# Optimization experiments

Measured on AMD Instinct MI355X. Metric: run time of the kernel, lower is better.

Reference implementation:

```python
import jax, jax.numpy as jnp
import numpy as np

DELTA_V = 0.5
DELTA_D = 1.5
ALPHA = 1.0
BETA = 1.0
GAMMA = 0.001
K = 33  # label ids 0..32; 0 = background (ignored)
EPS = 1e-12


def setup_inputs() -> dict:
    key = jax.random.key(0)
    k1, k2 = jax.random.split(key)
    B, N, E = 8, 65536, 32
    embeddings = jax.random.normal(k1, (B, N, E), dtype=jnp.float32)
    labels = jax.random.randint(k2, (B, N), 0, K)
    return {"embeddings": embeddings, "labels": labels}


def reference(embeddings, labels):
    B, N, E = embeddings.shape
    dt = embeddings.dtype
    seg = (labels + jnp.arange(B)[:, None] * K).reshape(-1)  # (B*N,)

    # segment mean -> per-instance centers (B, K, E)
    sums = jax.ops.segment_sum(embeddings.reshape(B * N, E), seg, num_segments=B * K).reshape(B, K, E)
    counts = jax.ops.segment_sum(jnp.ones((B * N,), dtype=dt), seg, num_segments=B * K).reshape(B, K)
    centers = sums / jnp.maximum(counts, 1.0)[..., None]

    present = counts > 0
    present = present.at[:, 0].set(False)  # drop background label 0
    presf = present.astype(dt)
    n_inst = presf.sum(axis=1)  # (B,)

    # ---- variance term: per-point hinge distance to own center, segment-mean ----
    c_per_point = centers[jnp.arange(B)[:, None], labels]  # (B, N, E) gather
    d2 = ((embeddings - c_per_point) ** 2).sum(-1)
    dist = jnp.sqrt(jnp.maximum(d2, EPS))
    hinge = jnp.where(labels > 0, jnp.maximum(dist - DELTA_V, 0.0), 0.0)
    per_inst_sum = jax.ops.segment_sum(hinge.reshape(-1), seg, num_segments=B * K).reshape(B, K)
    per_inst_mean = per_inst_sum / jnp.maximum(counts, 1.0)
    variance_term = (per_inst_mean * presf).sum(1) / jnp.maximum(n_inst, 1.0)

    # ---- distance term: pairwise hinge between present instance centers ----
    diff2 = ((centers[:, :, None, :] - centers[:, None, :, :]) ** 2).sum(-1)  # (B,K,K)
    upper = jnp.triu(jnp.ones((K, K), dtype=bool), 1)[None]
    pair_valid = present[:, :, None] & present[:, None, :] & upper
    cd = jnp.sqrt(jnp.maximum(jnp.where(pair_valid, diff2, 1.0), EPS))
    pair_hinge = jnp.maximum(2.0 * DELTA_D - cd, 0.0) * pair_valid.astype(dt)
    n_pairs = n_inst * (n_inst - 1.0) * 0.5
    distance_term = pair_hinge.sum((1, 2)) / jnp.maximum(n_pairs, 1.0)

    # ---- regularization: mean L2 norm of present centers ----
    c_norm = jnp.sqrt(jnp.maximum((centers ** 2).sum(-1), EPS))
    reg_term = (c_norm * presf).sum(1) / jnp.maximum(n_inst, 1.0)

    per_batch = ALPHA * variance_term + BETA * distance_term + GAMMA * reg_term
    per_batch = jnp.where(n_inst > 0, per_batch, 0.0)
    return per_batch.sum() / B
```

## Files before the change

### kernel.cpp

```cpp
#include <hip/hip_runtime.h>
#include <math.h>

#define KC 33
#define ED 32
#define KE (KC * ED)
#define PAD 33

#define BPB_A 64
#define TPA 128
#define NSLOT 8
#define BPB_H 128
#define TPH 256


__global__ void k_zero(float* __restrict__ ws, int n, float* __restrict__ out) {
    int i = blockIdx.x * blockDim.x + threadIdx.x;
    if (i < n) ws[i] = 0.f;
    if (i == 0) out[0] = 0.f;
}

__global__ __launch_bounds__(256) void k_accum(const float* __restrict__ emb,
                                               const int* __restrict__ lab,
                                               float* __restrict__ sums,
                                               float* __restrict__ counts, int N) {
    __shared__ float s_tile[TPA * PAD];
    __shared__ float s_priv[NSLOT * KE];
    __shared__ int   s_lab[TPA];
    __shared__ float s_hist[2 * KC];
    int t = threadIdx.x;
    for (int i = t; i < NSLOT * KE; i += 256) s_priv[i] = 0.f;
    if (t < 2 * KC) s_hist[t] = 0.f;

    int b     = blockIdx.x / BPB_A;
    int blk   = blockIdx.x % BPB_A;
    int chunk = N / BPB_A;
    int e     = t & 31;
    int slot  = t >> 5;
    size_t pbase = (size_t)b * N + (size_t)blk * chunk;
    const int NT = chunk / TPA;

    const float4* g4 = (const float4*)(emb + pbase * ED);
    float4 r0 = g4[t], r1 = g4[t + 256], r2 = g4[t + 512], r3 = g4[t + 768];
    int rl = 0;
    if (t < TPA) rl = lab[pbase + t];
    __syncthreads();

    for (int tb = 0; tb < NT; tb++) {
        {
            int f, p, m;
            f = t;        p = f >> 3; m = (f & 7) * 4;
            { float* d = &s_tile[PAD * p + m]; d[0]=r0.x; d[1]=r0.y; d[2]=r0.z; d[3]=r0.w; }
            f = t + 256;  p = f >> 3; m = (f & 7) * 4;
            { float* d = &s_tile[PAD * p + m]; d[0]=r1.x; d[1]=r1.y; d[2]=r1.z; d[3]=r1.w; }
            f = t + 512;  p = f >> 3; m = (f & 7) * 4;
            { float* d = &s_tile[PAD * p + m]; d[0]=r2.x; d[1]=r2.y; d[2]=r2.z; d[3]=r2.w; }
            f = t + 768;  p = f >> 3; m = (f & 7) * 4;
            { float* d = &s_tile[PAD * p + m]; d[0]=r3.x; d[1]=r3.y; d[2]=r3.z; d[3]=r3.w; }
        }
        if (t < TPA) {
            s_lab[t] = rl;
            atomicAdd(&s_hist[(t >> 6) * KC + rl], 1.f);
        }
        __syncthreads();

        if (tb + 1 < NT) {
            const float4* gn = (const float4*)(emb + (pbase + (size_t)(tb + 1) * TPA) * ED);
            r0 = gn[t]; r1 = gn[t + 256]; r2 = gn[t + 512]; r3 = gn[t + 768];
            if (t < TPA) rl = lab[pbase + (size_t)(tb + 1) * TPA + t];
        }

        float* priv = &s_priv[slot * KE];
#pragma unroll
        for (int st = 0; st < TPA / NSLOT; st++) {
            int pt = st * NSLOT + slot;
            float x = s_tile[pt * PAD + e];
            int   k = s_lab[pt];
            priv[k * ED + e] += x;
        }
        __syncthreads();
    }

    for (int i = t; i < KE; i += 256) {
        float v = 0.f;
#pragma unroll
        for (int s = 0; s < NSLOT; s++) v += s_priv[s * KE + i];
        atomicAdd(&sums[(size_t)b * KE + i], v);
    }
    if (t < KC)
        atomicAdd(&counts[b * KC + t], s_hist[t] + s_hist[KC + t]);
}

__global__ __launch_bounds__(256) void k_hinge(const float* __restrict__ emb,
                                               const int* __restrict__ lab,
                                               const float* __restrict__ sums,
                                               const float* __restrict__ counts,
                                               float* __restrict__ var,
                                               unsigned* __restrict__ done,
                                               float* __restrict__ out,
                                               int N, int B) {
    __shared__ float s_tile[TPH * PAD];
    __shared__ float s_ctr[KC * PAD];
    __shared__ float s_cnt[KC];
    __shared__ float s_inv[KC];
    __shared__ int   s_prs[KC];
    __shared__ float s_reg[KC];
    __shared__ int   s_lab[TPH];
    __shared__ float s_red[4];
    __shared__ float s_red2[256];
    __shared__ int   s_last;
    int t     = threadIdx.x;
    int b     = blockIdx.x / BPB_H;
    int blk   = blockIdx.x % BPB_H;
    int chunk = N / BPB_H;
    size_t pbase = (size_t)b * N + (size_t)blk * chunk;
    const int NT = chunk / TPH;

    const float4* g4 = (const float4*)(emb + pbase * ED);
    float4 r0 = g4[t],        r1 = g4[t + 256],  r2 = g4[t + 512],  r3 = g4[t + 768];
    float4 r4 = g4[t + 1024], r5 = g4[t + 1280], r6 = g4[t + 1536], r7 = g4[t + 1792];
    int rl = lab[pbase + t];

    if (t < KC) {
        float c = counts[b * KC + t];
        s_cnt[t] = fmaxf(c, 1.f);
        int p = (t > 0 && c > 0.f) ? 1 : 0;
        s_inv[t] = p ? 1.f / fmaxf(c, 1.f) : 0.f;
        s_prs[t] = p;
    }
    __syncthreads();
    for (int i = t; i < KE; i += 256) {
        int k = i >> 5, e = i & 31;
        s_ctr[k * PAD + e] = sums[(size_t)b * KE + i] / s_cnt[k];
    }

    float hs = 0.f;
    for (int tb = 0; tb < NT; tb++) {
        {
            int f, p, m;
            f = t;         p = f >> 3; m = (f & 7) * 4;
            { float* d = &s_tile[PAD * p + m]; d[0]=r0.x; d[1]=r0.y; d[2]=r0.z; d[3]=r0.w; }
            f = t + 256;   p = f >> 3; m = (f & 7) * 4;
            { float* d = &s_tile[PAD * p + m]; d[0]=r1.x; d[1]=r1.y; d[2]=r1.z; d[3]=r1.w; }
            f = t + 512;   p = f >> 3; m = (f & 7) * 4;
            { float* d = &s_tile[PAD * p + m]; d[0]=r2.x; d[1]=r2.y; d[2]=r2.z; d[3]=r2.w; }
            f = t + 768;   p = f >> 3; m = (f & 7) * 4;
            { float* d = &s_tile[PAD * p + m]; d[0]=r3.x; d[1]=r3.y; d[2]=r3.z; d[3]=r3.w; }
            f = t + 1024;  p = f >> 3; m = (f & 7) * 4;
            { float* d = &s_tile[PAD * p + m]; d[0]=r4.x; d[1]=r4.y; d[2]=r4.z; d[3]=r4.w; }
            f = t + 1280;  p = f >> 3; m = (f & 7) * 4;
            { float* d = &s_tile[PAD * p + m]; d[0]=r5.x; d[1]=r5.y; d[2]=r5.z; d[3]=r5.w; }
            f = t + 1536;  p = f >> 3; m = (f & 7) * 4;
            { float* d = &s_tile[PAD * p + m]; d[0]=r6.x; d[1]=r6.y; d[2]=r6.z; d[3]=r6.w; }
            f = t + 1792;  p = f >> 3; m = (f & 7) * 4;
            { float* d = &s_tile[PAD * p + m]; d[0]=r7.x; d[1]=r7.y; d[2]=r7.z; d[3]=r7.w; }
        }
        s_lab[t] = rl;
        __syncthreads();

        if (tb + 1 < NT) {
            const float4* gn = (const float4*)(emb + (pbase + (size_t)(tb + 1) * TPH) * ED);
            r0 = gn[t];        r1 = gn[t + 256];  r2 = gn[t + 512];  r3 = gn[t + 768];
            r4 = gn[t + 1024]; r5 = gn[t + 1280]; r6 = gn[t + 1536]; r7 = gn[t + 1792];
            rl = lab[pbase + (size_t)(tb + 1) * TPH + t];
        }

        int   k  = s_lab[t];
        float iv = s_inv[k];
        const float* xr = &s_tile[t * PAD];
        const float* cr = &s_ctr[k * PAD];
        float d2 = 0.f;
#pragma unroll
        for (int j = 0; j < ED; j++) {
            float d = xr[j] - cr[j];
            d2 = fmaf(d, d, d2);
        }
        float dist = sqrtf(fmaxf(d2, 1e-12f));
        hs += fmaxf(dist - 0.5f, 0.f) * iv;
        __syncthreads();
    }

    hs += __shfl_xor(hs, 1);  hs += __shfl_xor(hs, 2);  hs += __shfl_xor(hs, 4);
    hs += __shfl_xor(hs, 8);  hs += __shfl_xor(hs, 16); hs += __shfl_xor(hs, 32);
    if ((t & 63) == 0) s_red[t >> 6] = hs;
    __syncthreads();
    if (t == 0) {
        atomicAdd(&var[b], s_red[0] + s_red[1] + s_red[2] + s_red[3]);
        __threadfence();
        unsigned old = atomicAdd(&done[b], 1u);
        s_last = (old == (unsigned)(BPB_H - 1)) ? 1 : 0;
    }
    __syncthreads();
    if (!s_last) return;

    __threadfence();
    if (t < KC) {
        float n2 = 0.f;
        for (int e2 = 0; e2 < ED; e2++) { float c = s_ctr[t * PAD + e2]; n2 += c * c; }
        s_reg[t] = s_prs[t] ? sqrtf(fmaxf(n2, 1e-12f)) : 0.f;
    }
    __syncthreads();

    float psum = 0.f;
    for (int q = t; q < KC * KC; q += 256) {
        int i = q / KC, j = q % KC;
        if (i < j && s_prs[i] && s_prs[j]) {
            float d2 = 0.f;
            for (int e2 = 0; e2 < ED; e2++) {
                float d = s_ctr[i * PAD + e2] - s_ctr[j * PAD + e2];
                d2 += d * d;
            }
            float cd = sqrtf(fmaxf(d2, 1e-12f));
            psum += fmaxf(3.0f - cd, 0.f);
        }
    }
    s_red2[t] = psum;
    __syncthreads();
    for (int s = 128; s > 0; s >>= 1) {
        if (t < s) s_red2[t] += s_red2[t + s];
        __syncthreads();
    }

    if (t == 0) {
        float vb = atomicAdd(&var[b], 0.f);
        float reg = 0.f; int n = 0;
        for (int k = 0; k < KC; k++) { reg += s_reg[k]; n += s_prs[k]; }
        float nf = (float)n;
        float variance_term = vb / fmaxf(nf, 1.f);
        float npairs = nf * (nf - 1.f) * 0.5f;
        float distance_term = s_red2[0] / fmaxf(npairs, 1.f);
        float reg_term = reg / fmaxf(nf, 1.f);
        float pb = variance_term + distance_term + 0.001f * reg_term;
        if (n == 0) pb = 0.f;
        atomicAdd(out, pb / (float)B);
    }
}

extern "C" void kernel_launch(void* const* d_in, const int* in_sizes, int n_in,
                              void* d_out, int out_size, void* d_ws, size_t ws_size,
                              hipStream_t stream) {
    const float* emb = (const float*)d_in[0];
    const int*   lab = (const int*)d_in[1];
    float* out = (float*)d_out;

    const int B = 8;
    const int N = in_sizes[1] / B;

    float*    sums   = (float*)d_ws;
    float*    counts = sums + (size_t)B * KE;
    float*    var    = counts + (size_t)B * KC;
    unsigned* done   = (unsigned*)(var + B);

    int zn = B * KE + B * KC + B + B;
    k_zero<<<(zn + 255) / 256, 256, 0, stream>>>((float*)d_ws, zn, out);
    k_accum<<<B * BPB_A, 256, 0, stream>>>(emb, lab, sums, counts, N);
    k_hinge<<<B * BPB_H, 256, 0, stream>>>(emb, lab, sums, counts, var, done, out, N, B);
}
```

Measured before the change: 147.9 us.

## Fuse accumulation and hinge kernels with per-batch grid barrier and reload

Merges the segment-sum kernel and the hinge/loss kernel into one persistent-style kernel. Each block accumulates its chunk, signals a per-batch ready counter, spin-waits until all 64 blocks of that batch finish, then computes the hinge over the same chunk, which it reloads from global memory and which is likely L2-resident. Labels are kept in registers across both phases. This removes one launch and the separate cold pass over the embeddings, but relies on all 512 blocks being co-resident to avoid deadlock and adds spin-wait synchronisation.

```diff
diff --git a/kernel.cpp b/kernel.cpp
--- a/kernel.cpp
+++ b/kernel.cpp
@@ -6,11 +6,11 @@
 #define KE (KC * ED)
 #define PAD 33
 
-#define BPB_A 64
+#define BPB 64
 #define TPA 128
+#define NT 8
 #define NSLOT 8
-#define BPB_H 128
-#define TPH 256
+#define NT2 4
 
 
 __global__ void k_zero(float* __restrict__ ws, int n, float* __restrict__ out) {
@@ -19,30 +19,43 @@
     if (i == 0) out[0] = 0.f;
 }
 
-__global__ __launch_bounds__(256) void k_accum(const float* __restrict__ emb,
-                                               const int* __restrict__ lab,
-                                               float* __restrict__ sums,
-                                               float* __restrict__ counts, int N) {
-    __shared__ float s_tile[TPA * PAD];
+__global__ __launch_bounds__(256, 2) void k_fused(
+        const float* __restrict__ emb, const int* __restrict__ lab,
+        float* __restrict__ sums, float* __restrict__ counts,
+        float* __restrict__ var, unsigned* __restrict__ done,
+        unsigned* __restrict__ ready, float* __restrict__ out,
+        int N, int B) {
+    __shared__ float s_tile[2 * TPA * PAD];
     __shared__ float s_priv[NSLOT * KE];
-    __shared__ int   s_lab[TPA];
     __shared__ float s_hist[2 * KC];
+    __shared__ int   s_lab[2 * TPA];
+    __shared__ float s_ctr[KC * PAD];
+    __shared__ float s_cnt[KC];
+    __shared__ float s_inv[KC];
+    __shared__ int   s_prs[KC];
+    __shared__ float s_reg[KC];
+    __shared__ float s_red[4];
+    __shared__ float s_red2[256];
+    __shared__ int   s_last;
     int t = threadIdx.x;
+    int b = blockIdx.x / BPB;
+    int blk = blockIdx.x % BPB;
+    int chunk = N / BPB;
+    int e = t & 31, slot = t >> 3 >> 2;
+    slot = t >> 5;
+    size_t pbase = (size_t)b * N + (size_t)blk * chunk;
+    const float4* g4 = (const float4*)(emb + pbase * ED);
+
     for (int i = t; i < NSLOT * KE; i += 256) s_priv[i] = 0.f;
     if (t < 2 * KC) s_hist[t] = 0.f;
 
-    int b     = blockIdx.x / BPB_A;
-    int blk   = blockIdx.x % BPB_A;
-    int chunk = N / BPB_A;
-    int e     = t & 31;
-    int slot  = t >> 5;
-    size_t pbase = (size_t)b * N + (size_t)blk * chunk;
-    const int NT = chunk / TPA;
-
-    const float4* g4 = (const float4*)(emb + pbase * ED);
+    int rl_all[NT];
+    if (t < TPA) {
+#pragma unroll
+        for (int tb = 0; tb < NT; tb++) rl_all[tb] = lab[pbase + tb * TPA + t];
+    }
+
     float4 r0 = g4[t], r1 = g4[t + 256], r2 = g4[t + 512], r3 = g4[t + 768];
-    int rl = 0;
-    if (t < TPA) rl = lab[pbase + t];
     __syncthreads();
 
     for (int tb = 0; tb < NT; tb++) {
@@ -58,15 +71,14 @@
             { float* d = &s_tile[PAD * p + m]; d[0]=r3.x; d[1]=r3.y; d[2]=r3.z; d[3]=r3.w; }
         }
         if (t < TPA) {
-            s_lab[t] = rl;
-            atomicAdd(&s_hist[(t >> 6) * KC + rl], 1.f);
+            s_lab[t] = rl_all[tb];
+            atomicAdd(&s_hist[(t >> 6) * KC + rl_all[tb]], 1.f);
         }
         __syncthreads();
 
         if (tb + 1 < NT) {
             const float4* gn = (const float4*)(emb + (pbase + (size_t)(tb + 1) * TPA) * ED);
             r0 = gn[t]; r1 = gn[t + 256]; r2 = gn[t + 512]; r3 = gn[t + 768];
-            if (t < TPA) rl = lab[pbase + (size_t)(tb + 1) * TPA + t];
         }
 
         float* priv = &s_priv[slot * KE];
@@ -74,12 +86,11 @@
         for (int st = 0; st < TPA / NSLOT; st++) {
             int pt = st * NSLOT + slot;
             float x = s_tile[pt * PAD + e];
-            int   k = s_lab[pt];
+            int k = s_lab[pt];
             priv[k * ED + e] += x;
         }
         __syncthreads();
     }
-
     for (int i = t; i < KE; i += 256) {
         float v = 0.f;
 #pragma unroll
@@ -88,40 +99,20 @@
     }
     if (t < KC)
         atomicAdd(&counts[b * KC + t], s_hist[t] + s_hist[KC + t]);
-}
-
-__global__ __launch_bounds__(256) void k_hinge(const float* __restrict__ emb,
-                                               const int* __restrict__ lab,
-                                               const float* __restrict__ sums,
-                                               const float* __restrict__ counts,
-                                               float* __restrict__ var,
-                                               unsigned* __restrict__ done,
-                                               float* __restrict__ out,
-                                               int N, int B) {
-    __shared__ float s_tile[TPH * PAD];
-    __shared__ float s_ctr[KC * PAD];
-    __shared__ float s_cnt[KC];
-    __shared__ float s_inv[KC];
-    __shared__ int   s_prs[KC];
-    __shared__ float s_reg[KC];
-    __shared__ int   s_lab[TPH];
-    __shared__ float s_red[4];
-    __shared__ float s_red2[256];
-    __shared__ int   s_last;
-    int t     = threadIdx.x;
-    int b     = blockIdx.x / BPB_H;
-    int blk   = blockIdx.x % BPB_H;
-    int chunk = N / BPB_H;
-    size_t pbase = (size_t)b * N + (size_t)blk * chunk;
-    const int NT = chunk / TPH;
-
-    const float4* g4 = (const float4*)(emb + pbase * ED);
-    float4 r0 = g4[t],        r1 = g4[t + 256],  r2 = g4[t + 512],  r3 = g4[t + 768];
-    float4 r4 = g4[t + 1024], r5 = g4[t + 1280], r6 = g4[t + 1536], r7 = g4[t + 1792];
-    int rl = lab[pbase + t];
+    __syncthreads();
+
+    if (t == 0) {
+        __threadfence();
+        atomicAdd(&ready[b], 1u);
+        while (__hip_atomic_load(&ready[b], __ATOMIC_ACQUIRE,
+                                 __HIP_MEMORY_SCOPE_AGENT) < (unsigned)BPB)
+            __builtin_amdgcn_s_sleep(8);
+    }
+    __syncthreads();
 
     if (t < KC) {
-        float c = counts[b * KC + t];
+        float c = __hip_atomic_load(&counts[b * KC + t], __ATOMIC_RELAXED,
+                                    __HIP_MEMORY_SCOPE_AGENT);
         s_cnt[t] = fmaxf(c, 1.f);
         int p = (t > 0 && c > 0.f) ? 1 : 0;
         s_inv[t] = p ? 1.f / fmaxf(c, 1.f) : 0.f;
@@ -129,39 +120,46 @@
     }
     __syncthreads();
     for (int i = t; i < KE; i += 256) {
-        int k = i >> 5, e = i & 31;
-        s_ctr[k * PAD + e] = sums[(size_t)b * KE + i] / s_cnt[k];
-    }
+        int k = i >> 5, e2 = i & 31;
+        float sv = __hip_atomic_load(&sums[(size_t)b * KE + i], __ATOMIC_RELAXED,
+                                     __HIP_MEMORY_SCOPE_AGENT);
+        s_ctr[k * PAD + e2] = sv / s_cnt[k];
+    }
+
+    float4 x0 = g4[t],        x1 = g4[t + 256],  x2 = g4[t + 512],  x3 = g4[t + 768];
+    float4 x4 = g4[t + 1024], x5 = g4[t + 1280], x6 = g4[t + 1536], x7 = g4[t + 1792];
 
     float hs = 0.f;
-    for (int tb = 0; tb < NT; tb++) {
+    for (int i2 = 0; i2 < NT2; i2++) {
         {
             int f, p, m;
             f = t;         p = f >> 3; m = (f & 7) * 4;
-            { float* d = &s_tile[PAD * p + m]; d[0]=r0.x; d[1]=r0.y; d[2]=r0.z; d[3]=r0.w; }
+            { float* d = &s_tile[PAD * p + m]; d[0]=x0.x; d[1]=x0.y; d[2]=x0.z; d[3]=x0.w; }
             f = t + 256;   p = f >> 3; m = (f & 7) * 4;
-            { float* d = &s_tile[PAD * p + m]; d[0]=r1.x; d[1]=r1.y; d[2]=r1.z; d[3]=r1.w; }
+            { float* d = &s_tile[PAD * p + m]; d[0]=x1.x; d[1]=x1.y; d[2]=x1.z; d[3]=x1.w; }
             f = t + 512;   p = f >> 3; m = (f & 7) * 4;
-            { float* d = &s_tile[PAD * p + m]; d[0]=r2.x; d[1]=r2.y; d[2]=r2.z; d[3]=r2.w; }
+            { float* d = &s_tile[PAD * p + m]; d[0]=x2.x; d[1]=x2.y; d[2]=x2.z; d[3]=x2.w; }
             f = t + 768;   p = f >> 3; m = (f & 7) * 4;
-            { float* d = &s_tile[PAD * p + m]; d[0]=r3.x; d[1]=r3.y; d[2]=r3.z; d[3]=r3.w; }
+            { float* d = &s_tile[PAD * p + m]; d[0]=x3.x; d[1]=x3.y; d[2]=x3.z; d[3]=x3.w; }
             f = t + 1024;  p = f >> 3; m = (f & 7) * 4;
-            { float* d = &s_tile[PAD * p + m]; d[0]=r4.x; d[1]=r4.y; d[2]=r4.z; d[3]=r4.w; }
+            { float* d = &s_tile[PAD * p + m]; d[0]=x4.x; d[1]=x4.y; d[2]=x4.z; d[3]=x4.w; }
             f = t + 1280;  p = f >> 3; m = (f & 7) * 4;
-            { float* d = &s_tile[PAD * p + m]; d[0]=r5.x; d[1]=r5.y; d[2]=r5.z; d[3]=r5.w; }
+            { float* d = &s_tile[PAD * p + m]; d[0]=x5.x; d[1]=x5.y; d[2]=x5.z; d[3]=x5.w; }
             f = t + 1536;  p = f >> 3; m = (f & 7) * 4;
-            { float* d = &s_tile[PAD * p + m]; d[0]=r6.x; d[1]=r6.y; d[2]=r6.z; d[3]=r6.w; }
+            { float* d = &s_tile[PAD * p + m]; d[0]=x6.x; d[1]=x6.y; d[2]=x6.z; d[3]=x6.w; }
             f = t + 1792;  p = f >> 3; m = (f & 7) * 4;
-            { float* d = &s_tile[PAD * p + m]; d[0]=r7.x; d[1]=r7.y; d[2]=r7.z; d[3]=r7.w; }
-        }
-        s_lab[t] = rl;
-        __syncthreads();
-
-        if (tb + 1 < NT) {
-            const float4* gn = (const float4*)(emb + (pbase + (size_t)(tb + 1) * TPH) * ED);
-            r0 = gn[t];        r1 = gn[t + 256];  r2 = gn[t + 512];  r3 = gn[t + 768];
-            r4 = gn[t + 1024]; r5 = gn[t + 1280]; r6 = gn[t + 1536]; r7 = gn[t + 1792];
-            rl = lab[pbase + (size_t)(tb + 1) * TPH + t];
+            { float* d = &s_tile[PAD * p + m]; d[0]=x7.x; d[1]=x7.y; d[2]=x7.z; d[3]=x7.w; }
+        }
+        if (t < TPA) {
+            s_lab[t]       = rl_all[2 * i2];
+            s_lab[t + TPA] = rl_all[2 * i2 + 1];
+        }
+        __syncthreads();
+
+        if (i2 + 1 < NT2) {
+            const float4* gn = g4 + (size_t)(i2 + 1) * 2048;
+            x0 = gn[t];        x1 = gn[t + 256];  x2 = gn[t + 512];  x3 = gn[t + 768];
+            x4 = gn[t + 1024]; x5 = gn[t + 1280]; x6 = gn[t + 1536]; x7 = gn[t + 1792];
         }
 
         int   k  = s_lab[t];
@@ -187,7 +185,7 @@
         atomicAdd(&var[b], s_red[0] + s_red[1] + s_red[2] + s_red[3]);
         __threadfence();
         unsigned old = atomicAdd(&done[b], 1u);
-        s_last = (old == (unsigned)(BPB_H - 1)) ? 1 : 0;
+        s_last = (old == (unsigned)(BPB - 1)) ? 1 : 0;
     }
     __syncthreads();
     if (!s_last) return;
@@ -242,16 +240,17 @@
     const int*   lab = (const int*)d_in[1];
     float* out = (float*)d_out;
 
-    const int B = 8;
-    const int N = in_sizes[1] / B;
+    int B = 8;
+    int N = in_sizes[1] / B;
 
     float*    sums   = (float*)d_ws;
     float*    counts = sums + (size_t)B * KE;
     float*    var    = counts + (size_t)B * KC;
     unsigned* done   = (unsigned*)(var + B);
-
-    int zn = B * KE + B * KC + B + B;
+    unsigned* ready  = done + B;
+
+    int zn = B * KE + B * KC + B + B + B;
     k_zero<<<(zn + 255) / 256, 256, 0, stream>>>((float*)d_ws, zn, out);
-    k_accum<<<B * BPB_A, 256, 0, stream>>>(emb, lab, sums, counts, N);
-    k_hinge<<<B * BPB_H, 256, 0, stream>>>(emb, lab, sums, counts, var, done, out, N, B);
+    k_fused<<<B * BPB, 256, 0, stream>>>(emb, lab, sums, counts, var, done,
+                                         ready, out, N, B);
 }
```

Result: slower. 181.9 us (+23.0%).
